# Performance work log

Measured on AMD Instinct MI355X. Metric: run time of the kernel, lower is better.

## Reference

```python
import jax, jax.numpy as jnp
import numpy as np

SEQ_LEN = 2048
WIN = 2
LAYERS = 3
D_MODEL = 512
TDA_DIM = 7
TDA_WEIGHT = 0.3


def _nan0(x):
    return jnp.where(jnp.isnan(x), jnp.zeros_like(x), x)


def _tda_features(x):
    # x: [B, T, D] -> [B, 7]; vectorized version of the per-(b,d) stats loop
    B, T, D = x.shape
    mean = x.mean(axis=1)                                  # [B, D]
    std = x.std(axis=1, ddof=1)                            # torch.std is unbiased
    mn = x.min(axis=1)
    mx = x.max(axis=1)
    idx = jnp.arange(T, dtype=x.dtype)
    xc = x - mean[:, None, :]
    ic = idx - idx.mean()
    trend = _nan0(jnp.einsum('btd,t->bd', xc, ic) /
                  jnp.sqrt((xc * xc).sum(axis=1) * (ic * ic).sum()))
    # lag-1 autocorrelation via corrcoef of (x[:-1], x[1:])
    a = x[:, :-1, :]; b = x[:, 1:, :]
    ac = a - a.mean(axis=1, keepdims=True)
    bc = b - b.mean(axis=1, keepdims=True)
    autocorr = _nan0((ac * bc).sum(axis=1) /
                     jnp.sqrt((ac * ac).sum(axis=1) * (bc * bc).sum(axis=1)))
    # spectral centroid over first T//2 bins of |fft|^2 (== |rfft|^2 there)
    half = T // 2
    ps = jnp.abs(jnp.fft.rfft(x, axis=1)[:, :half, :]) ** 2  # [B, half, D]
    centroid = _nan0(jnp.einsum('btd,t->bd', ps, idx[:half]) / ps.sum(axis=1))
    feats = jnp.stack([mean, std, mn, mx, trend, autocorr, centroid], axis=-1)  # [B, D, 7]
    return feats.mean(axis=1)  # mean over channels -> [B, 7]


def _freq_interp(x, src_len, tgt_len):
    # x: [B, D, src_len] -> [B, D, tgt_len]; zero-pad/truncate in rfft domain
    xf = jnp.fft.rfft(x, axis=2)
    tgt_f = tgt_len // 2 + 1
    copy = min(xf.shape[2], tgt_f)
    out_f = jnp.zeros(x.shape[:2] + (tgt_f,), dtype=xf.dtype).at[:, :, :copy].set(xf[:, :, :copy])
    return jnp.fft.irfft(out_f, n=tgt_len, axis=2) * (src_len / tgt_len)


def _forward(levels, w1, b1, w2, b2, inj_w, inj_b):
    tda = _tda_features(levels[0])                              # [B, 7]
    h = jnp.maximum(tda @ w1 + b1, 0.0)
    attn = jax.nn.sigmoid(h @ w2 + b2)[:, None, :]              # [B, 1, D]
    rev = levels[::-1]
    n = len(rev)
    out_low, out_high = rev[0], rev[1]
    outs = [out_low]
    num_inj = LAYERS + 1
    for i in range(n - 1):
        src = SEQ_LEN // WIN ** (LAYERS - i)
        tgt = SEQ_LEN // WIN ** (LAYERS - i - 1)
        res = _freq_interp(out_low.transpose(0, 2, 1), src, tgt).transpose(0, 2, 1)
        left = (out_high - res) * attn
        safe_idx = (n - i - 2) % num_inj
        left = left + TDA_WEIGHT * (tda @ inj_w[safe_idx] + inj_b[safe_idx])[:, None, :]
        out_low = out_high
        if i + 2 <= n - 1:
            out_high = rev[i + 2]
        outs.append(left)
    return tuple(outs[::-1])


def setup_inputs() -> dict:
    key = jax.random.key(0)
    ks = jax.random.split(key, 20)
    B = 32
    inp = {}
    for l in range(LAYERS + 1):
        T = SEQ_LEN // WIN ** l
        inp[f'level{l}'] = jax.random.normal(ks[l], (B, T, D_MODEL), dtype=jnp.float32)
    s7 = 1.0 / np.sqrt(TDA_DIM)
    sd = 1.0 / np.sqrt(D_MODEL)
    inp['w1'] = jax.random.normal(ks[4], (TDA_DIM, D_MODEL), dtype=jnp.float32) * s7
    inp['b1'] = jnp.zeros((D_MODEL,), dtype=jnp.float32)
    inp['w2'] = jax.random.normal(ks[5], (D_MODEL, D_MODEL), dtype=jnp.float32) * sd
    inp['b2'] = jnp.zeros((D_MODEL,), dtype=jnp.float32)
    for j in range(LAYERS + 1):
        inp[f'wi{j}'] = jax.random.normal(ks[6 + j], (TDA_DIM, D_MODEL), dtype=jnp.float32) * s7
        inp[f'bi{j}'] = jnp.zeros((D_MODEL,), dtype=jnp.float32)
    return inp


def reference(level0, level1, level2, level3, w1, b1, w2, b2,
              wi0, bi0, wi1, bi1, wi2, bi2, wi3, bi3):
    levels = [level0, level1, level2, level3]
    inj_w = [wi0, wi1, wi2, wi3]
    inj_b = [bi0, bi1, bi2, bi3]
    return _forward(levels, w1, b1, w2, b2, inj_w, inj_b)
```

## Files before the change

kernel.cpp:

```cpp
#include <hip/hip_runtime.h>
#include <math.h>

constexpr int B  = 32;
constexpr int T0 = 2048;
constexpr int D  = 512;

constexpr size_t OFF_PART = 0;
constexpr size_t OFF_ATTN = OFF_PART + (size_t)B * 64 * 8;
constexpr size_t OFF_INJ  = OFF_ATTN + (size_t)B * D;

typedef float nfloat4 __attribute__((ext_vector_type(4)));

template<int LO>
__device__ __forceinline__ void wredt_add(float& v) {
  #pragma unroll
  for (int off = 32; off >= LO; off >>= 1) v += __shfl_down(v, off);
}
template<int LO>
__device__ __forceinline__ void wredt_min(float& v) {
  #pragma unroll
  for (int off = 32; off >= LO; off >>= 1) v = fminf(v, __shfl_down(v, off));
}
template<int LO>
__device__ __forceinline__ void wredt_max(float& v) {
  #pragma unroll
  for (int off = 32; off >= LO; off >>= 1) v = fmaxf(v, __shfl_down(v, off));
}
__device__ __forceinline__ void wred_add(float& v) { wredt_add<4>(v); }

__device__ __forceinline__ void nt_store4(float* p, float4 v) {
  nfloat4 nv;
  nv.x = v.x; nv.y = v.y; nv.z = v.z; nv.w = v.w;
  __builtin_nontemporal_store(nv, (nfloat4*)p);
}

__device__ __forceinline__ float4 cadd(float4 a, float4 b) {
  return make_float4(a.x+b.x, a.y+b.y, a.z+b.z, a.w+b.w);
}
__device__ __forceinline__ float4 csub(float4 a, float4 b) {
  return make_float4(a.x-b.x, a.y-b.y, a.z-b.z, a.w-b.w);
}
__device__ __forceinline__ float4 cmul(float4 v, float2 w) {
  return make_float4(v.x*w.x - v.y*w.y, v.x*w.y + v.y*w.x,
                     v.z*w.x - v.w*w.y, v.z*w.y + v.w*w.x);
}
__device__ __forceinline__ float4 cmulc(float4 v, float2 w) {
  return make_float4(v.x*w.x + v.y*w.y, v.y*w.x - v.x*w.y,
                     v.z*w.x + v.w*w.y, v.w*w.x - v.z*w.y);
}
__device__ __forceinline__ float4 cmul_mi(float4 v) {
  return make_float4(v.y, -v.x, v.w, -v.z);
}
__device__ __forceinline__ float4 cmul_pi(float4 v) {
  return make_float4(-v.y, v.x, -v.w, v.z);
}

#define R8C 0.70710678118654752f

__device__ __forceinline__ void r8_fwd(float4 x[8], float2 tA, float2 tB, float2 tC) {
  float4 a0 = cadd(x[0], x[4]), a1 = cadd(x[1], x[5]);
  float4 a2 = cadd(x[2], x[6]), a3 = cadd(x[3], x[7]);
  float4 b0 = cmul(csub(x[0], x[4]), tA);
  float4 b1 = cmul(cmul(csub(x[1], x[5]), tA), make_float2(R8C, -R8C));
  float4 b2 = cmul_mi(cmul(csub(x[2], x[6]), tA));
  float4 b3 = cmul(cmul(csub(x[3], x[7]), tA), make_float2(-R8C, -R8C));
  float4 p0 = cadd(a0, a2), p1 = cmul(csub(a0, a2), tB);
  float4 p2 = cadd(a1, a3), p3 = cmul_mi(cmul(csub(a1, a3), tB));
  x[0] = cadd(p0, p2); x[1] = cmul(csub(p0, p2), tC);
  x[2] = cadd(p1, p3); x[3] = cmul(csub(p1, p3), tC);
  float4 q0 = cadd(b0, b2), q1 = cmul(csub(b0, b2), tB);
  float4 q2 = cadd(b1, b3), q3 = cmul_mi(cmul(csub(b1, b3), tB));
  x[4] = cadd(q0, q2); x[5] = cmul(csub(q0, q2), tC);
  x[6] = cadd(q1, q3); x[7] = cmul(csub(q1, q3), tC);
}

__device__ __forceinline__ void r8_inv(float4 x[8], float2 wA, float2 wB, float2 wC) {
  float4 t1 = cmulc(x[1], wA); float4 u0 = cadd(x[0], t1), u1 = csub(x[0], t1);
  float4 t3 = cmulc(x[3], wA); float4 u2 = cadd(x[2], t3), u3 = csub(x[2], t3);
  float4 t5 = cmulc(x[5], wA); float4 u4 = cadd(x[4], t5), u5 = csub(x[4], t5);
  float4 t7 = cmulc(x[7], wA); float4 u6 = cadd(x[6], t7), u7 = csub(x[6], t7);
  float4 s2 = cmulc(u2, wB), s3 = cmul_pi(cmulc(u3, wB));
  float4 y0 = cadd(u0, s2), y1 = cadd(u1, s3), y2 = csub(u0, s2), y3 = csub(u1, s3);
  float4 s6 = cmulc(u6, wB), s7 = cmul_pi(cmulc(u7, wB));
  float4 y4 = cadd(u4, s6), y5 = cadd(u5, s7), y6 = csub(u4, s6), y7 = csub(u5, s7);
  float4 c0 = cmulc(y4, wC);
  float4 c1 = cmul(cmulc(y5, wC), make_float2(R8C, R8C));
  float4 c2 = cmul_pi(cmulc(y6, wC));
  float4 c3 = cmul(cmulc(y7, wC), make_float2(-R8C, R8C));
  x[0] = cadd(y0, c0); x[1] = cadd(y1, c1); x[2] = cadd(y2, c2); x[3] = cadd(y3, c3);
  x[4] = csub(y0, c0); x[5] = csub(y1, c1); x[6] = csub(y2, c2); x[7] = csub(y3, c3);
}

__global__ __launch_bounds__(512) void k_tda(const float* __restrict__ x,
                                              float* __restrict__ part) {
  __shared__ float4 buf[T0 * 2];
  __shared__ float2 tw[1024];
  __shared__ float perd[8][8];
  float* scr = (float*)tw;
  const int tid  = threadIdx.x;
  const int L = blockIdx.x + 64 * blockIdx.y;
  const int m = (L >> 3) & 1;
  const int q = (L & 7) | ((L >> 4) << 3);
  const int eb = (q & 31) * 2 + m;
  const int b  = q >> 5;
  const int f    = tid & 1;
  const int rIdx = tid >> 1;
  const int lane = tid & 63;
  const int wv   = tid >> 6;
  const float* base = x + (size_t)b * T0 * D + eb * 8 + f * 4;

  float4 s1 = {0,0,0,0}, s2 = {0,0,0,0}, st = {0,0,0,0};
  float4 mn = {INFINITY,INFINITY,INFINITY,INFINITY};
  float4 mx = {-INFINITY,-INFINITY,-INFINITY,-INFINITY};
  #pragma unroll
  for (int u = 0; u < 8; ++u) {
    int t = rIdx + 256 * u;
    float4 v = *(const float4*)&base[(size_t)t * D];
    buf[t * 2 + f] = v;
    float tf = (float)t;
    s1.x += v.x; s1.y += v.y; s1.z += v.z; s1.w += v.w;
    s2.x = fmaf(v.x,v.x,s2.x); s2.y = fmaf(v.y,v.y,s2.y);
    s2.z = fmaf(v.z,v.z,s2.z); s2.w = fmaf(v.w,v.w,s2.w);
    st.x = fmaf(tf,v.x,st.x); st.y = fmaf(tf,v.y,st.y);
    st.z = fmaf(tf,v.z,st.z); st.w = fmaf(tf,v.w,st.w);
    mn.x = fminf(mn.x,v.x); mn.y = fminf(mn.y,v.y); mn.z = fminf(mn.z,v.z); mn.w = fminf(mn.w,v.w);
    mx.x = fmaxf(mx.x,v.x); mx.y = fmaxf(mx.y,v.y); mx.z = fmaxf(mx.z,v.z); mx.w = fmaxf(mx.w,v.w);
  }
  __syncthreads();
  float4 cc = {0,0,0,0};
  #pragma unroll
  for (int u = 0; u < 8; ++u) {
    int t = rIdx + 256 * u;
    if (t < T0 - 1) {
      float4 a = buf[t * 2 + f];
      float4 nb = buf[(t + 1) * 2 + f];
      cc.x = fmaf(a.x,nb.x,cc.x); cc.y = fmaf(a.y,nb.y,cc.y);
      cc.z = fmaf(a.z,nb.z,cc.z); cc.w = fmaf(a.w,nb.w,cc.w);
    }
  }
  wredt_add<2>(s1.x); wredt_add<2>(s1.y); wredt_add<2>(s1.z); wredt_add<2>(s1.w);
  wredt_add<2>(s2.x); wredt_add<2>(s2.y); wredt_add<2>(s2.z); wredt_add<2>(s2.w);
  wredt_add<2>(st.x); wredt_add<2>(st.y); wredt_add<2>(st.z); wredt_add<2>(st.w);
  wredt_add<2>(cc.x); wredt_add<2>(cc.y); wredt_add<2>(cc.z); wredt_add<2>(cc.w);
  wredt_min<2>(mn.x); wredt_min<2>(mn.y); wredt_min<2>(mn.z); wredt_min<2>(mn.w);
  wredt_max<2>(mx.x); wredt_max<2>(mx.y); wredt_max<2>(mx.z); wredt_max<2>(mx.w);
  if (lane < 2) {
    float* p = scr + ((size_t)wv * 2 + f) * 24;
    p[0]=s1.x; p[1]=s2.x; p[2]=st.x; p[3]=cc.x; p[4]=mn.x; p[5]=mx.x;
    p[6]=s1.y; p[7]=s2.y; p[8]=st.y; p[9]=cc.y; p[10]=mn.y; p[11]=mx.y;
    p[12]=s1.z; p[13]=s2.z; p[14]=st.z; p[15]=cc.z; p[16]=mn.z; p[17]=mx.z;
    p[18]=s1.w; p[19]=s2.w; p[20]=st.w; p[21]=cc.w; p[22]=mn.w; p[23]=mx.w;
  }
  __syncthreads();
  if (tid < 8) {
    const int dl = tid;
    const int fq = dl >> 2, c = dl & 3;
    float S1=0.f, S2=0.f, St=0.f, C=0.f, MN=INFINITY, MX=-INFINITY;
    for (int w = 0; w < 8; ++w) {
      const float* p = scr + ((size_t)w * 2 + fq) * 24 + c * 6;
      S1 += p[0]; S2 += p[1]; St += p[2]; C += p[3];
      MN = fminf(MN, p[4]); MX = fmaxf(MX, p[5]);
    }
    const float x0 = ((const float*)buf)[dl];
    const float xl = ((const float*)buf)[(size_t)(T0 - 1) * 8 + dl];
    const float Tf = (float)T0;
    const float mean = S1 / Tf;
    const float sxx  = S2 - S1 * S1 / Tf;
    const float stdv = sqrtf(fmaxf(sxx / (Tf - 1.f), 0.f));
    const float tbar = (Tf - 1.f) * 0.5f;
    const float Sic  = Tf * (Tf * Tf - 1.f) / 12.f;
    float trend = (St - tbar * S1) / sqrtf(sxx * Sic);
    if (isnan(trend)) trend = 0.f;
    const float na = Tf - 1.f;
    const float Sa = S1 - xl, Sb = S1 - x0;
    const float an  = C - Sa * Sb / na;
    const float sa2 = (S2 - xl * xl) - Sa * Sa / na;
    const float sb2 = (S2 - x0 * x0) - Sb * Sb / na;
    float ac = an / sqrtf(sa2 * sb2);
    if (isnan(ac)) ac = 0.f;
    perd[dl][0] = mean; perd[dl][1] = stdv; perd[dl][2] = MN;
    perd[dl][3] = MX;   perd[dl][4] = trend; perd[dl][5] = ac;
  }
  __syncthreads();

  for (int k = tid; k < 1024; k += 512) {
    float sw, cw;
    sincosf(-(float)M_PI * (float)k * (1.0f / 1024.0f), &sw, &cw);
    tw[k] = make_float2(cw, sw);
  }
  __syncthreads();

  for (int stg = 0; stg < 9; stg += 3) {
    const int qsh = 8 - stg;
    const int Q = 1 << qsh;
    int pp = tid & 1;
    int gi = tid >> 1;
    int j3 = gi & (Q - 1);
    int g  = gi >> qsh;
    int bs = (g << (qsh + 3)) + j3;
    float2 tA = tw[j3 << stg];
    float2 tB = tw[j3 << (stg + 1)];
    float2 tC = tw[j3 << (stg + 2)];
    float4 xx[8];
    #pragma unroll
    for (int mm = 0; mm < 8; ++mm) xx[mm] = buf[(bs + mm * Q) * 2 + pp];
    r8_fwd(xx, tA, tB, tC);
    #pragma unroll
    for (int mm = 0; mm < 8; ++mm) buf[(bs + mm * Q) * 2 + pp] = xx[mm];
    __syncthreads();
  }
  #pragma unroll
  for (int it = 0; it < 2; ++it) {
    int sl = it * 512 + tid;
    int pp = sl & 1;
    int qi = sl >> 1;
    int bs = qi << 2;
    float4 x0 = buf[bs*2+pp], x1 = buf[(bs+1)*2+pp];
    float4 x2 = buf[(bs+2)*2+pp], x3 = buf[(bs+3)*2+pp];
    float4 u0 = cadd(x0, x2);
    float4 t2 = csub(x0, x2);
    float4 u1 = cadd(x1, x3);
    float4 t3 = cmul_mi(csub(x1, x3));
    buf[bs*2+pp]     = cadd(u0, u1);
    buf[(bs+1)*2+pp] = csub(u0, u1);
    buf[(bs+2)*2+pp] = cadd(t2, t3);
    buf[(bs+3)*2+pp] = csub(t2, t3);
  }
  __syncthreads();

  float4 num = {0,0,0,0}, den = {0,0,0,0};
  #pragma unroll
  for (int it = 0; it < 4; ++it) {
    int sl = it * 512 + tid;
    int pp = sl & 1;
    int k = sl >> 1;
    int p1 = __brev((unsigned)k) >> 21;
    int p2 = __brev((unsigned)((T0 - k) & (T0 - 1))) >> 21;
    float4 zk = buf[p1 * 2 + pp];
    float4 zm = buf[p2 * 2 + pp];
    float kf = (float)k;
    float arx = 0.5f*(zk.x+zm.x), ary = 0.5f*(zk.y-zm.y);
    float brx = 0.5f*(zk.y+zm.y), bry = 0.5f*(zm.x-zk.x);
    float pa = arx*arx + ary*ary, pb = brx*brx + bry*bry;
    num.x = fmaf(kf, pa, num.x); den.x += pa;
    num.y = fmaf(kf, pb, num.y); den.y += pb;
    arx = 0.5f*(zk.z+zm.z); ary = 0.5f*(zk.w-zm.w);
    brx = 0.5f*(zk.w+zm.w); bry = 0.5f*(zm.z-zk.z);
    pa = arx*arx + ary*ary; pb = brx*brx + bry*bry;
    num.z = fmaf(kf, pa, num.z); den.z += pa;
    num.w = fmaf(kf, pb, num.w); den.w += pb;
  }
  wredt_add<2>(num.x); wredt_add<2>(num.y); wredt_add<2>(num.z); wredt_add<2>(num.w);
  wredt_add<2>(den.x); wredt_add<2>(den.y); wredt_add<2>(den.z); wredt_add<2>(den.w);
  if (lane < 2) {
    float* p = scr + ((size_t)wv * 2 + f) * 8;
    p[0]=num.x; p[1]=num.y; p[2]=num.z; p[3]=num.w;
    p[4]=den.x; p[5]=den.y; p[6]=den.z; p[7]=den.w;
  }
  __syncthreads();
  if (tid < 8) {
    const int dl = tid;
    const int fq = dl >> 2, c = dl & 3;
    float N = 0.f, Dn = 0.f;
    for (int w = 0; w < 8; ++w) {
      const float* p = scr + ((size_t)w * 2 + fq) * 8;
      N += p[c]; Dn += p[4 + c];
    }
    float cent = N / Dn;
    if (isnan(cent)) cent = 0.f;
    perd[dl][6] = cent;
  }
  __syncthreads();
  if (tid < 7) {
    float s = 0.f;
    #pragma unroll
    for (int dl = 0; dl < 8; ++dl) s += perd[dl][tid];
    part[((size_t)b * 64 + eb) * 8 + tid] = s;
  }
}

__global__ __launch_bounds__(512) void k_weights(const float* __restrict__ part,
    const float* __restrict__ w1, const float* __restrict__ b1,
    const float* __restrict__ w2, const float* __restrict__ b2,
    const float* __restrict__ wi0, const float* __restrict__ bi0,
    const float* __restrict__ wi1, const float* __restrict__ bi1,
    const float* __restrict__ wi2, const float* __restrict__ bi2,
    float* __restrict__ attn, float* __restrict__ inj) {
  const int b = blockIdx.x;
  const int j = threadIdx.x;
  __shared__ float td[7];
  __shared__ float h[512];
  if (j < 7) {
    float s = 0.f;
    for (int w = 0; w < 64; ++w) s += part[((size_t)b * 64 + w) * 8 + j];
    td[j] = s * (1.0f / (float)D);
  }
  __syncthreads();
  float a = b1[j];
  #pragma unroll
  for (int f = 0; f < 7; ++f) a = fmaf(td[f], w1[f * D + j], a);
  h[j] = fmaxf(a, 0.0f);
  __syncthreads();
  float a2 = b2[j];
  for (int k = 0; k < D; ++k) a2 = fmaf(h[k], w2[k * D + j], a2);
  attn[(size_t)b * D + j] = 1.0f / (1.0f + expf(-a2));
  const float* wis[3] = {wi0, wi1, wi2};
  const float* bis[3] = {bi0, bi1, bi2};
  #pragma unroll
  for (int l = 0; l < 3; ++l) {
    float ai = bis[l][j];
    #pragma unroll
    for (int f = 0; f < 7; ++f) ai = fmaf(td[f], wis[l][f * D + j], ai);
    inj[(size_t)l * B * D + (size_t)b * D + j] = 0.3f * ai;
  }
}

template<int S, int NT, bool COPY>
__global__ __launch_bounds__(NT) void k_interp(const float* __restrict__ low,
                                                const float* __restrict__ high,
                                                const float* __restrict__ attn,
                                                const float* __restrict__ inj,
                                                float* __restrict__ out,
                                                float* __restrict__ copy_out) {
  constexpr int LOG2S = (S == 1024) ? 10 : (S == 512) ? 9 : 8;
  constexpr int WAVES = NT / 64;
  constexpr int RPT   = S / (NT / 4);
  constexpr int R8IT  = S / 2;
  __shared__ float4 buf[S * 4];
  __shared__ float2 tw[S];
  __shared__ float4 scrA[WAVES][4];
  __shared__ float4 Zh4[4];
  const int tid  = threadIdx.x;
  const int L = blockIdx.x + 32 * blockIdx.y;
  const int m = (L >> 3) & 1;
  const int q = (L & 7) | ((L >> 4) << 3);
  const int eb = (q & 15) * 2 + m;
  const int b  = q >> 4;
  const int f    = tid & 3;
  const int rIdx = tid >> 2;
  const int lane = tid & 63;
  const int wv   = tid >> 6;
  const int d0   = eb * 16;

  const float* lowb  = low  + (size_t)b * S * D + d0 + 4 * f;
  const float* highb = high + (size_t)b * (2 * S) * D + d0 + 4 * f;
  float*       outb  = out  + (size_t)b * (2 * S) * D + d0 + 4 * f;
  float*       cpb   = COPY ? copy_out + (size_t)b * S * D + d0 + 4 * f : nullptr;

  float4 zreg[RPT];
  float4 acc = {0,0,0,0};
  #pragma unroll
  for (int u = 0; u < RPT; ++u) {
    int t = rIdx + (NT / 4) * u;
    float4 v = *(const float4*)&lowb[(size_t)t * D];
    zreg[u] = v;
    buf[t * 4 + f] = v;
    if (COPY) nt_store4(&cpb[(size_t)t * D], v);
    acc.x += v.x; acc.y += v.y; acc.z += v.z; acc.w += v.w;
  }
  if (rIdx & 1) { acc.x = -acc.x; acc.y = -acc.y; acc.z = -acc.z; acc.w = -acc.w; }
  for (int k = tid; k < S; k += NT) {
    float sw, cw;
    sincosf(-(float)M_PI * (float)k * (1.0f / (float)S), &sw, &cw);
    tw[k] = make_float2(cw, sw);
  }
  wred_add(acc.x); wred_add(acc.y); wred_add(acc.z); wred_add(acc.w);
  if (lane < 4) scrA[wv][f] = acc;
  __syncthreads();
  if (tid < 4) {
    float4 s = scrA[0][tid];
    for (int w = 1; w < WAVES; ++w) {
      float4 qv = scrA[w][tid];
      s.x += qv.x; s.y += qv.y; s.z += qv.z; s.w += qv.w;
    }
    Zh4[tid] = s;
  }
  __syncthreads();

  const float inv4S = 1.0f / (4.0f * (float)S);
  const float4 at4 = *(const float4*)&attn[(size_t)b * D + d0 + 4 * f];
  const float4 in4 = *(const float4*)&inj [(size_t)b * D + d0 + 4 * f];
  float4 Zs = Zh4[f];
  Zs.x *= inv4S; Zs.y *= inv4S; Zs.z *= inv4S; Zs.w *= inv4S;

  for (int stg = 0; stg + 2 < LOG2S; stg += 3) {
    const int qsh = LOG2S - 3 - stg;
    const int Q = 1 << qsh;
    #pragma unroll
    for (int it = 0; it < (R8IT + NT - 1) / NT; ++it) {
      int sl = it * NT + tid;
      if (sl < R8IT) {
        int pp = sl & 3;
        int gi = sl >> 2;
        int j3 = gi & (Q - 1);
        int g  = gi >> qsh;
        int bs = (g << (qsh + 3)) + j3;
        float2 tA = tw[j3 << (stg + 1)];
        float2 tB = tw[j3 << (stg + 2)];
        float2 tC = tw[j3 << (stg + 3)];
        float4 xx[8];
        #pragma unroll
        for (int mm = 0; mm < 8; ++mm) xx[mm] = buf[(bs + mm * Q) * 4 + pp];
        r8_fwd(xx, tA, tB, tC);
        #pragma unroll
        for (int mm = 0; mm < 8; ++mm) buf[(bs + mm * Q) * 4 + pp] = xx[mm];
      }
      __syncthreads();
    }
  }
  if (LOG2S % 3 == 1) {
    #pragma unroll
    for (int it = 0; it < (2 * S) / NT; ++it) {
      int sl = it * NT + tid;
      int pp = sl & 3;
      int bi = sl >> 2;
      int i = bi * 2;
      float4 a = buf[i * 4 + pp];
      float4 c4 = buf[(i + 1) * 4 + pp];
      buf[i * 4 + pp]       = cadd(a, c4);
      buf[(i + 1) * 4 + pp] = csub(a, c4);
    }
    __syncthreads();
  }
  if (LOG2S % 3 == 2) {
    #pragma unroll
    for (int it = 0; it < S / NT; ++it) {
      int sl = it * NT + tid;
      int pp = sl & 3;
      int qi = sl >> 2;
      int bs = qi << 2;
      float4 x0 = buf[bs*4+pp], x1 = buf[(bs+1)*4+pp];
      float4 x2 = buf[(bs+2)*4+pp], x3 = buf[(bs+3)*4+pp];
      float4 u0 = cadd(x0, x2);
      float4 t2 = csub(x0, x2);
      float4 u1 = cadd(x1, x3);
      float4 t3 = cmul_mi(csub(x1, x3));
      buf[bs*4+pp]     = cadd(u0, u1);
      buf[(bs+1)*4+pp] = csub(u0, u1);
      buf[(bs+2)*4+pp] = cadd(t2, t3);
      buf[(bs+3)*4+pp] = csub(t2, t3);
    }
    __syncthreads();
  }

  for (int stg = 0; stg + 2 < LOG2S; stg += 3) {
    const int h = 1 << stg;
    #pragma unroll
    for (int it = 0; it < (R8IT + NT - 1) / NT; ++it) {
      int sl = it * NT + tid;
      if (sl < R8IT) {
        int pp = sl & 3;
        int gi = sl >> 2;
        int j  = gi & (h - 1);
        int G  = gi >> stg;
        int bs = (G << (stg + 3)) + j;
        float2 wA = tw[j << (LOG2S - stg)];
        float2 wB = tw[j << (LOG2S - stg - 1)];
        float2 wC = tw[j << (LOG2S - stg - 2)];
        float4 xx[8];
        if (stg == 0) {
          #pragma unroll
          for (int mm = 0; mm < 8; ++mm) {
            int p = bs + mm;
            int k = __brev((unsigned)p) >> (32 - LOG2S);
            float2 w = tw[k];
            float sgn = (k < S / 2) ? 1.f : (k == S / 2) ? 0.f : -1.f;
            float4 v = cmulc(buf[p * 4 + pp], w);
            v.x *= sgn; v.y *= sgn; v.z *= sgn; v.w *= sgn;
            xx[mm] = v;
          }
        } else {
          #pragma unroll
          for (int mm = 0; mm < 8; ++mm) xx[mm] = buf[(bs + mm * h) * 4 + pp];
        }
        r8_inv(xx, wA, wB, wC);
        #pragma unroll
        for (int mm = 0; mm < 8; ++mm) buf[(bs + mm * h) * 4 + pp] = xx[mm];
      }
      __syncthreads();
    }
  }
  if (LOG2S % 3 == 1) {
    const int stg = LOG2S - 1;
    const int h = 1 << stg;
    #pragma unroll
    for (int it = 0; it < (2 * S) / NT; ++it) {
      int sl = it * NT + tid;
      int pp = sl & 3;
      int bi = sl >> 2;
      int j = bi & (h - 1);
      int g = bi >> stg;
      int i = (g << (stg + 1)) + j;
      float2 w = tw[j << (LOG2S - stg)];
      float4 a = buf[i * 4 + pp];
      float4 v = buf[(i + h) * 4 + pp];
      float4 t = cmulc(v, w);
      buf[i * 4 + pp]       = cadd(a, t);
      buf[(i + h) * 4 + pp] = csub(a, t);
    }
    __syncthreads();
  }
  if (LOG2S % 3 == 2) {
    const int stg = LOG2S - 2;
    const int h = 1 << stg;
    #pragma unroll
    for (int it = 0; it < S / NT; ++it) {
      int sl = it * NT + tid;
      int pp = sl & 3;
      int qi = sl >> 2;
      int j = qi & (h - 1);
      int g = qi >> stg;
      int bs = (g << (stg + 2)) + j;
      float2 wA = tw[j << (LOG2S - stg)];
      float2 wB = tw[j << (LOG2S - stg - 1)];
      float4 x0 = buf[bs * 4 + pp];
      float4 x1 = buf[(bs + h) * 4 + pp];
      float4 x2 = buf[(bs + 2 * h) * 4 + pp];
      float4 x3 = buf[(bs + 3 * h) * 4 + pp];
      float4 t1 = cmulc(x1, wA);
      float4 u0 = cadd(x0, t1), u1 = csub(x0, t1);
      float4 t3 = cmulc(x3, wA);
      float4 u2 = cadd(x2, t3), u3 = csub(x2, t3);
      float4 s2c = cmulc(u2, wB);
      float4 s3c = cmul_pi(cmulc(u3, wB));
      buf[bs * 4 + pp]           = cadd(u0, s2c);
      buf[(bs + h) * 4 + pp]     = cadd(u1, s3c);
      buf[(bs + 2 * h) * 4 + pp] = csub(u0, s2c);
      buf[(bs + 3 * h) * 4 + pp] = csub(u1, s3c);
    }
    __syncthreads();
  }

  #pragma unroll
  for (int u = 0; u < RPT; ++u) {
    int j = rIdx + (NT / 4) * u;
    float4 z = zreg[u];
    float sg = (j & 1) ? -1.f : 1.f;
    float4 res_e;
    res_e.x = fmaf(0.25f, z.x, sg * Zs.x);
    res_e.y = fmaf(0.25f, z.y, sg * Zs.y);
    res_e.z = fmaf(0.25f, z.z, sg * Zs.z);
    res_e.w = fmaf(0.25f, z.w, sg * Zs.w);
    float4 y = buf[j * 4 + f];
    float4 h0 = *(const float4*)&highb[(size_t)(2 * j) * D];
    float4 h1 = *(const float4*)&highb[(size_t)(2 * j + 1) * D];
    float4 o0, o1;
    o0.x = fmaf(h0.x - res_e.x, at4.x, in4.x);
    o0.y = fmaf(h0.y - res_e.y, at4.y, in4.y);
    o0.z = fmaf(h0.z - res_e.z, at4.z, in4.z);
    o0.w = fmaf(h0.w - res_e.w, at4.w, in4.w);
    o1.x = fmaf(h1.x - y.x * inv4S, at4.x, in4.x);
    o1.y = fmaf(h1.y - y.y * inv4S, at4.y, in4.y);
    o1.z = fmaf(h1.z - y.z * inv4S, at4.z, in4.z);
    o1.w = fmaf(h1.w - y.w * inv4S, at4.w, in4.w);
    nt_store4(&outb[(size_t)(2 * j) * D], o0);
    nt_store4(&outb[(size_t)(2 * j + 1) * D], o1);
  }
}

extern "C" void kernel_launch(void* const* d_in, const int* in_sizes, int n_in,
                              void* d_out, int out_size, void* d_ws, size_t ws_size,
                              hipStream_t stream) {
  const float* level0 = (const float*)d_in[0];
  const float* level1 = (const float*)d_in[1];
  const float* level2 = (const float*)d_in[2];
  const float* level3 = (const float*)d_in[3];
  const float* w1  = (const float*)d_in[4];
  const float* b1  = (const float*)d_in[5];
  const float* w2  = (const float*)d_in[6];
  const float* b2  = (const float*)d_in[7];
  const float* wi0 = (const float*)d_in[8];
  const float* bi0 = (const float*)d_in[9];
  const float* wi1 = (const float*)d_in[10];
  const float* bi1 = (const float*)d_in[11];
  const float* wi2 = (const float*)d_in[12];
  const float* bi2 = (const float*)d_in[13];

  float* ws   = (float*)d_ws;
  float* part = ws + OFF_PART;
  float* attn = ws + OFF_ATTN;
  float* inj  = ws + OFF_INJ;

  float* out0 = (float*)d_out;
  float* out1 = out0 + (size_t)B * 2048 * D;
  float* out2 = out1 + (size_t)B * 1024 * D;
  float* out3 = out2 + (size_t)B * 512 * D;

  k_tda<<<dim3(64, B), 512, 0, stream>>>(level0, part);
  k_weights<<<B, 512, 0, stream>>>(part, w1, b1, w2, b2, wi0, bi0, wi1, bi1, wi2, bi2,
                                   attn, inj);

  k_interp<1024, 512, false><<<dim3(32, B), 512, 0, stream>>>(
      level1, level0, attn, inj + 0ull * B * D, out0, nullptr);
  k_interp<512, 512, false><<<dim3(32, B), 512, 0, stream>>>(
      level2, level1, attn, inj + 1ull * B * D, out1, nullptr);
  k_interp<256, 256, true><<<dim3(32, B), 256, 0, stream>>>(
      level3, level2, attn, inj + 2ull * B * D, out2, out3);
}
```

Measured before the change: 257.8 us.

## Merge three interpolation kernels into a single launch

Replaces the three per-level interpolation launches with one kernel whose blocks dispatch on block index to the matching level's body. This removes two launch boundaries and lets the tail of one level overlap the next. In exchange, every block reserves the largest level's shared memory, and the smallest level now runs with 512 threads instead of 256, so some threads idle and occupancy drops for the smaller levels.

New measurement: 266.8 us. 1.03x slower.

```diff
diff --git a/kernel.cpp b/kernel.cpp
--- a/kernel.cpp
+++ b/kernel.cpp
@@ -315,25 +315,20 @@
   }
 }
 
-template<int S, int NT, bool COPY>
-__global__ __launch_bounds__(NT) void k_interp(const float* __restrict__ low,
-                                                const float* __restrict__ high,
-                                                const float* __restrict__ attn,
-                                                const float* __restrict__ inj,
-                                                float* __restrict__ out,
-                                                float* __restrict__ copy_out) {
+template<int S, bool COPY>
+__device__ __forceinline__ void interp_body(int bb,
+    const float* __restrict__ low, const float* __restrict__ high,
+    const float* __restrict__ attn, const float* __restrict__ inj,
+    float* __restrict__ out, float* __restrict__ copy_out,
+    float4* buf, float2* tw, float4 (*scrA)[4], float4* Zh4) {
+  constexpr int NT = 512;
   constexpr int LOG2S = (S == 1024) ? 10 : (S == 512) ? 9 : 8;
   constexpr int WAVES = NT / 64;
   constexpr int RPT   = S / (NT / 4);
   constexpr int R8IT  = S / 2;
-  __shared__ float4 buf[S * 4];
-  __shared__ float2 tw[S];
-  __shared__ float4 scrA[WAVES][4];
-  __shared__ float4 Zh4[4];
   const int tid  = threadIdx.x;
-  const int L = blockIdx.x + 32 * blockIdx.y;
-  const int m = (L >> 3) & 1;
-  const int q = (L & 7) | ((L >> 4) << 3);
+  const int m = (bb >> 3) & 1;
+  const int q = (bb & 7) | ((bb >> 4) << 3);
   const int eb = (q & 15) * 2 + m;
   const int b  = q >> 4;
   const int f    = tid & 3;
@@ -424,21 +419,23 @@
   }
   if (LOG2S % 3 == 2) {
     #pragma unroll
-    for (int it = 0; it < S / NT; ++it) {
+    for (int it = 0; it < (S + NT - 1) / NT; ++it) {
       int sl = it * NT + tid;
-      int pp = sl & 3;
-      int qi = sl >> 2;
-      int bs = qi << 2;
-      float4 x0 = buf[bs*4+pp], x1 = buf[(bs+1)*4+pp];
-      float4 x2 = buf[(bs+2)*4+pp], x3 = buf[(bs+3)*4+pp];
-      float4 u0 = cadd(x0, x2);
-      float4 t2 = csub(x0, x2);
-      float4 u1 = cadd(x1, x3);
-      float4 t3 = cmul_mi(csub(x1, x3));
-      buf[bs*4+pp]     = cadd(u0, u1);
-      buf[(bs+1)*4+pp] = csub(u0, u1);
-      buf[(bs+2)*4+pp] = cadd(t2, t3);
-      buf[(bs+3)*4+pp] = csub(t2, t3);
+      if (sl < S) {
+        int pp = sl & 3;
+        int qi = sl >> 2;
+        int bs = qi << 2;
+        float4 x0 = buf[bs*4+pp], x1 = buf[(bs+1)*4+pp];
+        float4 x2 = buf[(bs+2)*4+pp], x3 = buf[(bs+3)*4+pp];
+        float4 u0 = cadd(x0, x2);
+        float4 t2 = csub(x0, x2);
+        float4 u1 = cadd(x1, x3);
+        float4 t3 = cmul_mi(csub(x1, x3));
+        buf[bs*4+pp]     = cadd(u0, u1);
+        buf[(bs+1)*4+pp] = csub(u0, u1);
+        buf[(bs+2)*4+pp] = cadd(t2, t3);
+        buf[(bs+3)*4+pp] = csub(t2, t3);
+      }
     }
     __syncthreads();
   }
@@ -504,29 +501,31 @@
     const int stg = LOG2S - 2;
     const int h = 1 << stg;
     #pragma unroll
-    for (int it = 0; it < S / NT; ++it) {
+    for (int it = 0; it < (S + NT - 1) / NT; ++it) {
       int sl = it * NT + tid;
-      int pp = sl & 3;
-      int qi = sl >> 2;
-      int j = qi & (h - 1);
-      int g = qi >> stg;
-      int bs = (g << (stg + 2)) + j;
-      float2 wA = tw[j << (LOG2S - stg)];
-      float2 wB = tw[j << (LOG2S - stg - 1)];
-      float4 x0 = buf[bs * 4 + pp];
-      float4 x1 = buf[(bs + h) * 4 + pp];
-      float4 x2 = buf[(bs + 2 * h) * 4 + pp];
-      float4 x3 = buf[(bs + 3 * h) * 4 + pp];
-      float4 t1 = cmulc(x1, wA);
-      float4 u0 = cadd(x0, t1), u1 = csub(x0, t1);
-      float4 t3 = cmulc(x3, wA);
-      float4 u2 = cadd(x2, t3), u3 = csub(x2, t3);
-      float4 s2c = cmulc(u2, wB);
-      float4 s3c = cmul_pi(cmulc(u3, wB));
-      buf[bs * 4 + pp]           = cadd(u0, s2c);
-      buf[(bs + h) * 4 + pp]     = cadd(u1, s3c);
-      buf[(bs + 2 * h) * 4 + pp] = csub(u0, s2c);
-      buf[(bs + 3 * h) * 4 + pp] = csub(u1, s3c);
+      if (sl < S) {
+        int pp = sl & 3;
+        int qi = sl >> 2;
+        int j = qi & (h - 1);
+        int g = qi >> stg;
+        int bs = (g << (stg + 2)) + j;
+        float2 wA = tw[j << (LOG2S - stg)];
+        float2 wB = tw[j << (LOG2S - stg - 1)];
+        float4 x0 = buf[bs * 4 + pp];
+        float4 x1 = buf[(bs + h) * 4 + pp];
+        float4 x2 = buf[(bs + 2 * h) * 4 + pp];
+        float4 x3 = buf[(bs + 3 * h) * 4 + pp];
+        float4 t1 = cmulc(x1, wA);
+        float4 u0 = cadd(x0, t1), u1 = csub(x0, t1);
+        float4 t3 = cmulc(x3, wA);
+        float4 u2 = cadd(x2, t3), u3 = csub(x2, t3);
+        float4 s2c = cmulc(u2, wB);
+        float4 s3c = cmul_pi(cmulc(u3, wB));
+        buf[bs * 4 + pp]           = cadd(u0, s2c);
+        buf[(bs + h) * 4 + pp]     = cadd(u1, s3c);
+        buf[(bs + 2 * h) * 4 + pp] = csub(u0, s2c);
+        buf[(bs + 3 * h) * 4 + pp] = csub(u1, s3c);
+      }
     }
     __syncthreads();
   }
@@ -558,6 +557,29 @@
   }
 }
 
+__global__ __launch_bounds__(512) void k_interp_all(
+    const float* __restrict__ l0, const float* __restrict__ l1,
+    const float* __restrict__ l2, const float* __restrict__ l3,
+    const float* __restrict__ attn, const float* __restrict__ inj,
+    float* __restrict__ out0, float* __restrict__ out1,
+    float* __restrict__ out2, float* __restrict__ out3) {
+  __shared__ float4 buf[4096];
+  __shared__ float2 tw[1024];
+  __shared__ float4 scrA[8][4];
+  __shared__ float4 Zh4[4];
+  const int gb = blockIdx.x;
+  if (gb < 1024) {
+    interp_body<1024, false>(gb, l1, l0, attn, inj + 0ull * B * D, out0, nullptr,
+                             buf, tw, scrA, Zh4);
+  } else if (gb < 2048) {
+    interp_body<512, false>(gb - 1024, l2, l1, attn, inj + 1ull * B * D, out1,
+                            nullptr, buf, tw, scrA, Zh4);
+  } else {
+    interp_body<256, true>(gb - 2048, l3, l2, attn, inj + 2ull * B * D, out2,
+                           out3, buf, tw, scrA, Zh4);
+  }
+}
+
 extern "C" void kernel_launch(void* const* d_in, const int* in_sizes, int n_in,
                               void* d_out, int out_size, void* d_ws, size_t ws_size,
                               hipStream_t stream) {
@@ -589,11 +611,6 @@
   k_tda<<<dim3(64, B), 512, 0, stream>>>(level0, part);
   k_weights<<<B, 512, 0, stream>>>(part, w1, b1, w2, b2, wi0, bi0, wi1, bi1, wi2, bi2,
                                    attn, inj);
-
-  k_interp<1024, 512, false><<<dim3(32, B), 512, 0, stream>>>(
-      level1, level0, attn, inj + 0ull * B * D, out0, nullptr);
-  k_interp<512, 512, false><<<dim3(32, B), 512, 0, stream>>>(
-      level2, level1, attn, inj + 1ull * B * D, out1, nullptr);
-  k_interp<256, 256, true><<<dim3(32, B), 256, 0, stream>>>(
-      level3, level2, attn, inj + 2ull * B * D, out2, out3);
-}
+  k_interp_all<<<3072, 512, 0, stream>>>(level0, level1, level2, level3,
+                                         attn, inj, out0, out1, out2, out3);
+}
```
